# Kernel optimization log

Measured on AMD Instinct MI355X. Metric: run time of the kernel, lower is better.

Reference implementation:

```python
import jax, jax.numpy as jnp
import numpy as np

EPS = 1e-3  # kernel epsilon used in Performer generalized kernel
B, H, N, D, M = 1, 8, 1024, 64, 128  # batch, heads, seq, dim_heads, nb_features


def _gaussian_orthogonal_matrix(m, d, seed=0):
    # GaussianOrthogonalRandomMatrix with scaling=0: stacked QR blocks, rows
    # rescaled by chi-distributed norms of gaussian d-vectors.
    rng = np.random.default_rng(seed)
    blocks = []
    for _ in range(m // d):
        g = rng.standard_normal((d, d))
        qmat, _ = np.linalg.qr(g)
        blocks.append(qmat.T)
    proj = np.concatenate(blocks, axis=0)  # [m, d], orthonormal rows per block
    mult = np.linalg.norm(rng.standard_normal((m, d)), axis=1)  # chi norms
    return (mult[:, None] * proj).astype(np.float32)


def setup_inputs() -> dict:
    key = jax.random.key(0)
    kq, kk, kv = jax.random.split(key, 3)
    q = jax.random.normal(kq, (B, H, N, D), dtype=jnp.float32)
    k = jax.random.normal(kk, (B, H, N, D), dtype=jnp.float32)
    v = jax.random.normal(kv, (B, H, N, D), dtype=jnp.float32)
    proj = jnp.asarray(_gaussian_orthogonal_matrix(M, D))
    return {"q": q, "k": k, "v": v, "proj": proj}


def _generalized_kernel(x, proj):
    # kernel_fn(relu)( (x / d**0.25) @ proj^T ) + eps
    normalizer = 1.0 / (x.shape[-1] ** 0.25)
    xp = jnp.einsum('bhnd,md->bhnm', x * normalizer, proj)
    return jax.nn.relu(xp) + EPS


def reference(q, k, v, proj):
    qp = _generalized_kernel(q, proj)  # [B,H,N,M]
    kp = _generalized_kernel(k, proj)  # [B,H,N,M]
    # causal linear attention
    k_cumsum = jnp.cumsum(kp, axis=-2)                              # [B,H,N,M]
    context = jnp.einsum('bhnm,bhne->bhnme', kp, v)                 # [B,H,N,M,D]
    context = jnp.cumsum(context, axis=-3)                          # prefix sums over n
    context = context / k_cumsum[..., None]                         # normalize
    out = jnp.einsum('bhnme,bhnm->bhne', context, qp)               # [B,H,N,D]
    return out
```

## Files before the change

kernel.cpp:

```cpp
#include <hip/hip_runtime.h>

static constexpr int H = 8, N = 1024, D = 64, M = 128, CHUNK = 128, NC = 8;
static constexpr float EPS = 1e-3f;
static constexpr float NORM = 0.35355339059327373f;

typedef __attribute__((ext_vector_type(8))) short short8;
typedef __attribute__((ext_vector_type(4))) float f32x4;

__device__ inline unsigned short f2bf(float x) {
    unsigned u = __float_as_uint(x);
    return (unsigned short)((u + 0x7fffu + ((u >> 16) & 1u)) >> 16);
}
__device__ inline float bf2f(unsigned short u) {
    return __uint_as_float(((unsigned)u) << 16);
}
__device__ inline ushort4 pack4(float4 g) {
    return (ushort4){f2bf(g.x), f2bf(g.y), f2bf(g.z), f2bf(g.w)};
}

__global__ __launch_bounds__(512) void k_projg(const float* __restrict__ q,
                                               const float* __restrict__ k,
                                               const float* __restrict__ proj,
                                               const float* __restrict__ v,
                                               unsigned short* __restrict__ qpb,
                                               unsigned short* __restrict__ kpb,
                                               unsigned short* __restrict__ Gpb,
                                               float* __restrict__ kpart) {
    __shared__ __align__(16) short smem[30208];
    short* projb = smem;
    short* xb = smem + 9216;
    short* obuf = smem + 13824;
    short* kpT = smem + 22528;
    short* vT = smem + 27648;
    const int tid = threadIdx.x;
    const int rblk = blockIdx.x;
    const int h = blockIdx.y;
    const int rowbase = h * N + rblk * 32;
    const int lane = tid & 63, wv = tid >> 6;
    const int rt = wv & 3, mh = wv >> 2;
    const int fr = lane & 15, fq = lane >> 4;

    for (int i4 = tid; i4 < 2048; i4 += 512) {
        int m = i4 >> 4, dq = i4 & 15;
        *(ushort4*)&projb[m * 72 + dq * 4] = pack4(*(const float4*)&proj[i4 * 4]);
    }
    {
        int r = tid >> 4, dq = tid & 15;
        float4 g = *(const float4*)&q[(rowbase + r) * D + dq * 4];
        g.x *= NORM; g.y *= NORM; g.z *= NORM; g.w *= NORM;
        *(ushort4*)&xb[r * 72 + dq * 4] = pack4(g);
        float4 gk = *(const float4*)&k[(rowbase + r) * D + dq * 4];
        gk.x *= NORM; gk.y *= NORM; gk.z *= NORM; gk.w *= NORM;
        *(ushort4*)&xb[(32 + r) * 72 + dq * 4] = pack4(gk);
        int rv = tid & 31, e4 = (tid >> 5) * 4;
        float4 gv = *(const float4*)&v[(rowbase + rv) * D + e4];
        vT[(e4 + 0) * 40 + rv] = (short)f2bf(gv.x);
        vT[(e4 + 1) * 40 + rv] = (short)f2bf(gv.y);
        vT[(e4 + 2) * 40 + rv] = (short)f2bf(gv.z);
        vT[(e4 + 3) * 40 + rv] = (short)f2bf(gv.w);
    }
    __syncthreads();

    f32x4 accp[4];
#pragma unroll
    for (int i = 0; i < 4; i++) accp[i] = (f32x4){0.f, 0.f, 0.f, 0.f};
#pragma unroll
    for (int kt = 0; kt < 2; kt++) {
        short8 a = *(const short8*)&xb[(16 * rt + fr) * 72 + kt * 32 + fq * 8];
#pragma unroll
        for (int i = 0; i < 4; i++) {
            const int mt = mh * 4 + i;
            short8 bb = *(const short8*)&projb[(16 * mt + fr) * 72 + kt * 32 + fq * 8];
            accp[i] = __builtin_amdgcn_mfma_f32_16x16x32_bf16(a, bb, accp[i], 0, 0, 0);
        }
    }
#pragma unroll
    for (int i = 0; i < 4; i++) {
        const int mt = mh * 4 + i;
#pragma unroll
        for (int reg = 0; reg < 4; reg++) {
            const int r = 16 * rt + fq * 4 + reg;
            const int m = 16 * mt + fr;
            unsigned short bv = f2bf(fmaxf(accp[i][reg], 0.f) + EPS);
            obuf[r * 136 + m] = (short)bv;
            if (rt >= 2) kpT[m * 40 + (r - 32)] = (short)bv;
        }
    }
    __syncthreads();

    for (int i = tid; i < 2048; i += 512) {
        int r = i >> 5, cu = i & 31;
        ushort4 val = *(const ushort4*)&obuf[r * 136 + cu * 4];
        unsigned short* g = (r < 32) ? &qpb[(rowbase + r) * M + cu * 4]
                                     : &kpb[(rowbase + r - 32) * M + cu * 4];
        *(ushort4*)g = val;
    }
    const int gb = h * 32 + rblk;
    if (tid < 128) {
        float ks = 0.f;
#pragma unroll 8
        for (int r = 0; r < 32; r++) ks += bf2f((unsigned short)kpT[tid * 40 + r]);
        kpart[gb * M + tid] = ks;
    }
    __syncthreads();

    f32x4 gacc[4];
#pragma unroll
    for (int et = 0; et < 4; et++) gacc[et] = (f32x4){0.f, 0.f, 0.f, 0.f};
    {
        short8 a = *(const short8*)&kpT[(16 * wv + fr) * 40 + fq * 8];
#pragma unroll
        for (int et = 0; et < 4; et++) {
            short8 bb = *(const short8*)&vT[(16 * et + fr) * 40 + fq * 8];
            gacc[et] = __builtin_amdgcn_mfma_f32_16x16x32_bf16(a, bb, gacc[et], 0, 0, 0);
        }
    }
#pragma unroll
    for (int et = 0; et < 4; et++)
#pragma unroll
        for (int reg = 0; reg < 4; reg++) {
            const int m = 16 * wv + fq * 4 + reg;
            obuf[m * 68 + 16 * et + fr] = (short)f2bf(gacc[et][reg]);
        }
    __syncthreads();
    for (int i = tid; i < 2048; i += 512) {
        int m = i >> 4, e4 = (i & 15) * 4;
        *(ushort4*)&Gpb[(gb * M + m) * D + e4] = *(const ushort4*)&obuf[m * 68 + e4];
    }
}

__global__ __launch_bounds__(256) void k_prefix(const float* __restrict__ kpart,
                                                const unsigned short* __restrict__ Gpb,
                                                float* __restrict__ zpre,
                                                unsigned short* __restrict__ S0pre) {
    const int h = blockIdx.x >> 3, oct = blockIdx.x & 7;
    const int tid = threadIdx.x;
    const int eb = oct * 1024 + tid * 4;
    float a0 = 0.f, a1 = 0.f, a2 = 0.f, a3 = 0.f;
#pragma unroll
    for (int c = 0; c < 8; c++) {
        ushort4 w = {f2bf(a0), f2bf(a1), f2bf(a2), f2bf(a3)};
        *(ushort4*)&S0pre[(h * 8 + c) * (M * D) + eb] = w;
#pragma unroll
        for (int p = 0; p < 4; p++) {
            ushort4 g = *(const ushort4*)&Gpb[(h * 32 + c * 4 + p) * (M * D) + eb];
            a0 += bf2f(g.x);
            a1 += bf2f(g.y);
            a2 += bf2f(g.z);
            a3 += bf2f(g.w);
        }
    }
    if (oct == 0 && tid < 128) {
        float vals[32];
#pragma unroll
        for (int s = 0; s < 32; s++) vals[s] = kpart[(h * 32 + s) * M + tid];
        float z = 0.f;
#pragma unroll
        for (int s = 0; s < 32; s++) {
            zpre[(h * 32 + s) * M + tid] = z;
            z += vals[s];
        }
    }
}

__global__ __launch_bounds__(512) void k_attn(const unsigned short* __restrict__ qpb,
                                              const unsigned short* __restrict__ kpb,
                                              const float* __restrict__ zpre,
                                              const unsigned short* __restrict__ S0pre,
                                              const float* __restrict__ v,
                                              float* __restrict__ out) {
    __shared__ __align__(16) short smem[26112];
    short* bufA = smem;
    short* bufB = smem + 4352;
    short* bufC = smem + 21760;
    short* s0t = bufB;
    short* vT = bufB + 8704;
    const int tid = threadIdx.x;
    const int b = blockIdx.x;
    const int sub = blockIdx.y;
    const int h = b >> 3, c = 7 - (b & 7);
    const int chunkbase = h * N + c * CHUNK;
    const int rowstart = chunkbase + sub * 32;
    const int jrows = (sub + 1) * 32;
    const int lane = tid & 63, wv = tid >> 6;
    const int rt = wv & 1, js = wv >> 1;
    const int fr = lane & 15, fq = lane >> 4;

    float4 vpre[4];
#pragma unroll
    for (int t = 0; t < 4; t++) {
        const int i = tid + t * 512;
        const int j = i >> 4, e4 = (i & 15) * 4;
        vpre[t] = *(const float4*)&v[(chunkbase + j) * D + e4];
    }
    const int pm = tid >> 2, peb = (tid & 3) * 16;
    short8 s0a = *(const short8*)&S0pre[(h * 8 + c) * (M * D) + pm * D + peb];
    short8 s0b = *(const short8*)&S0pre[(h * 8 + c) * (M * D) + pm * D + peb + 8];
    float zinit = 0.f;
    if (tid < 128) zinit = zpre[(h * 32 + c * 4 + sub) * M + tid];

    {
        const unsigned int* src = (const unsigned int*)kpb;
        for (int i = tid; i < jrows * 64; i += 512) {
            int j = i >> 6, mu = i & 63;
            ((unsigned int*)&bufB[j * 136])[mu] = src[(chunkbase + j) * 64 + mu];
        }
        const unsigned int* srcq = (const unsigned int*)qpb;
        for (int i = tid; i < 2048; i += 512) {
            int r = i >> 6, mu = i & 63;
            ((unsigned int*)&bufC[r * 136])[mu] = srcq[(rowstart + r) * 64 + mu];
        }
    }
    __syncthreads();

    if (tid < 128) {
        const int m = tid;
        float z = zinit;
#pragma unroll 8
        for (int r = 0; r < 32; r++) {
            z += bf2f((unsigned short)bufB[(sub * 32 + r) * 136 + m]);
            bufA[r * 136 + m] = (short)f2bf(
                bf2f((unsigned short)bufC[r * 136 + m]) * __builtin_amdgcn_rcpf(z));
        }
    }
    __syncthreads();

    const int jtmax = 2 * sub + 2;
    f32x4 acc1[2];
    acc1[0] = (f32x4){0.f, 0.f, 0.f, 0.f};
    acc1[1] = (f32x4){0.f, 0.f, 0.f, 0.f};
#pragma unroll
    for (int kt = 0; kt < 4; kt++) {
        short8 a = *(const short8*)&bufA[(16 * rt + fr) * 136 + kt * 32 + fq * 8];
#pragma unroll
        for (int jl = 0; jl < 2; jl++) {
            const int jt = 2 * js + jl;
            if (jt < jtmax) {
                short8 bb =
                    *(const short8*)&bufB[(16 * jt + fr) * 136 + kt * 32 + fq * 8];
                acc1[jl] =
                    __builtin_amdgcn_mfma_f32_16x16x32_bf16(a, bb, acc1[jl], 0, 0, 0);
            }
        }
    }
    __syncthreads();

#pragma unroll
    for (int jl = 0; jl < 2; jl++) {
        const int jt = 2 * js + jl;
        if (jt < jtmax) {
            const int j = 16 * jt + fr;
#pragma unroll
            for (int reg = 0; reg < 4; reg++) {
                const int nloc = 16 * rt + fq * 4 + reg;
                float val = (j <= sub * 32 + nloc) ? acc1[jl][reg] : 0.f;
                bufC[nloc * 136 + j] = (short)f2bf(val);
            }
        }
    }
    {
#pragma unroll
        for (int j = 0; j < 8; j++) {
            s0t[(peb + j) * 136 + pm] = s0a[j];
            s0t[(peb + 8 + j) * 136 + pm] = s0b[j];
        }
    }
#pragma unroll
    for (int t = 0; t < 4; t++) {
        const int i = tid + t * 512;
        const int j = i >> 4, e4 = (i & 15) * 4;
        vT[(e4 + 0) * 136 + j] = (short)f2bf(vpre[t].x);
        vT[(e4 + 1) * 136 + j] = (short)f2bf(vpre[t].y);
        vT[(e4 + 2) * 136 + j] = (short)f2bf(vpre[t].z);
        vT[(e4 + 3) * 136 + j] = (short)f2bf(vpre[t].w);
    }
    __syncthreads();

    f32x4 acc2 = (f32x4){0.f, 0.f, 0.f, 0.f};
#pragma unroll
    for (int kt = 0; kt < 4; kt++) {
        short8 a = *(const short8*)&bufA[(16 * rt + fr) * 136 + kt * 32 + fq * 8];
        short8 bb = *(const short8*)&s0t[(16 * js + fr) * 136 + kt * 32 + fq * 8];
        acc2 = __builtin_amdgcn_mfma_f32_16x16x32_bf16(a, bb, acc2, 0, 0, 0);
    }
    const int ktmax = sub + 1;
    for (int kt = 0; kt < ktmax; kt++) {
        short8 a = *(const short8*)&bufC[(16 * rt + fr) * 136 + kt * 32 + fq * 8];
        short8 bb = *(const short8*)&vT[(16 * js + fr) * 136 + kt * 32 + fq * 8];
        acc2 = __builtin_amdgcn_mfma_f32_16x16x32_bf16(a, bb, acc2, 0, 0, 0);
    }

#pragma unroll
    for (int reg = 0; reg < 4; reg++) {
        out[(rowstart + 16 * rt + fq * 4 + reg) * D + 16 * js + fr] = acc2[reg];
    }
}

extern "C" void kernel_launch(void* const* d_in, const int* in_sizes, int n_in,
                              void* d_out, int out_size, void* d_ws, size_t ws_size,
                              hipStream_t stream) {
    const float* q = (const float*)d_in[0];
    const float* k = (const float*)d_in[1];
    const float* v = (const float*)d_in[2];
    const float* proj = (const float*)d_in[3];
    float* out = (float*)d_out;

    float* ws = (float*)d_ws;
    float* kpart = ws;
    unsigned short* qpb = (unsigned short*)(kpart + H * 32 * M);
    unsigned short* kpb = qpb + H * N * M;
    unsigned short* Gpb = kpb + H * N * M;
    float* zpre = (float*)(Gpb + H * 32 * M * D);
    unsigned short* S0pre = (unsigned short*)(zpre + H * 32 * M);

    k_projg<<<dim3(32, H), 512, 0, stream>>>(q, k, proj, v, qpb, kpb, Gpb,
                                             kpart);
    k_prefix<<<dim3(64), 256, 0, stream>>>(kpart, Gpb, zpre, S0pre);
    k_attn<<<dim3(H * NC, 4), 512, 0, stream>>>(qpb, kpb, zpre, S0pre, v, out);
}
```

Before: 81.16 us.

## Switch causal attention to 32-row chunks with per-subchunk state prefixes

The prefix kernel now emits a state prefix for every 32-row subchunk instead of every 128-row chunk. Each attention block then handles only its own 32 rows: a 32x32 intra-chunk causal product plus a state product, with no redundant loading of earlier rows within the chunk. This removes the uneven per-block work and the large key loads, at the cost of four times more S0pre prefix data written and read from global memory. The launch grid changes from 64x4 to 256 one-dimensional blocks.

```diff
diff --git a/kernel.cpp b/kernel.cpp
--- a/kernel.cpp
+++ b/kernel.cpp
@@ -1,6 +1,6 @@
 #include <hip/hip_runtime.h>
 
-static constexpr int H = 8, N = 1024, D = 64, M = 128, CHUNK = 128, NC = 8;
+static constexpr int H = 8, N = 1024, D = 64, M = 128;
 static constexpr float EPS = 1e-3f;
 static constexpr float NORM = 0.35355339059327373f;
 
@@ -137,18 +137,15 @@
     const int tid = threadIdx.x;
     const int eb = oct * 1024 + tid * 4;
     float a0 = 0.f, a1 = 0.f, a2 = 0.f, a3 = 0.f;
-#pragma unroll
-    for (int c = 0; c < 8; c++) {
+#pragma unroll 4
+    for (int s = 0; s < 32; s++) {
         ushort4 w = {f2bf(a0), f2bf(a1), f2bf(a2), f2bf(a3)};
-        *(ushort4*)&S0pre[(h * 8 + c) * (M * D) + eb] = w;
-#pragma unroll
-        for (int p = 0; p < 4; p++) {
-            ushort4 g = *(const ushort4*)&Gpb[(h * 32 + c * 4 + p) * (M * D) + eb];
-            a0 += bf2f(g.x);
-            a1 += bf2f(g.y);
-            a2 += bf2f(g.z);
-            a3 += bf2f(g.w);
-        }
+        *(ushort4*)&S0pre[(h * 32 + s) * (M * D) + eb] = w;
+        ushort4 g = *(const ushort4*)&Gpb[(h * 32 + s) * (M * D) + eb];
+        a0 += bf2f(g.x);
+        a1 += bf2f(g.y);
+        a2 += bf2f(g.z);
+        a3 += bf2f(g.w);
     }
     if (oct == 0 && tid < 128) {
         float vals[32];
@@ -169,48 +166,51 @@
                                               const unsigned short* __restrict__ S0pre,
                                               const float* __restrict__ v,
                                               float* __restrict__ out) {
-    __shared__ __align__(16) short smem[26112];
-    short* bufA = smem;
-    short* bufB = smem + 4352;
-    short* bufC = smem + 21760;
-    short* s0t = bufB;
-    short* vT = bufB + 8704;
+    __shared__ __align__(16) short smem[25600];
+    short* bufW = smem;
+    short* bufK = smem + 4352;
+    short* bufQ = smem + 8704;
+    short* s0t  = smem + 13056;
+    short* vT   = smem + 21760;
+    short* bufP = smem + 24320;
     const int tid = threadIdx.x;
     const int b = blockIdx.x;
-    const int sub = blockIdx.y;
-    const int h = b >> 3, c = 7 - (b & 7);
-    const int chunkbase = h * N + c * CHUNK;
-    const int rowstart = chunkbase + sub * 32;
-    const int jrows = (sub + 1) * 32;
+    const int h = b >> 5, s = b & 31;
+    const int rowstart = h * N + s * 32;
     const int lane = tid & 63, wv = tid >> 6;
     const int rt = wv & 1, js = wv >> 1;
     const int fr = lane & 15, fq = lane >> 4;
 
-    float4 vpre[4];
-#pragma unroll
-    for (int t = 0; t < 4; t++) {
-        const int i = tid + t * 512;
-        const int j = i >> 4, e4 = (i & 15) * 4;
-        vpre[t] = *(const float4*)&v[(chunkbase + j) * D + e4];
-    }
-    const int pm = tid >> 2, peb = (tid & 3) * 16;
-    short8 s0a = *(const short8*)&S0pre[(h * 8 + c) * (M * D) + pm * D + peb];
-    short8 s0b = *(const short8*)&S0pre[(h * 8 + c) * (M * D) + pm * D + peb + 8];
-    float zinit = 0.f;
-    if (tid < 128) zinit = zpre[(h * 32 + c * 4 + sub) * M + tid];
-
-    {
-        const unsigned int* src = (const unsigned int*)kpb;
-        for (int i = tid; i < jrows * 64; i += 512) {
-            int j = i >> 6, mu = i & 63;
-            ((unsigned int*)&bufB[j * 136])[mu] = src[(chunkbase + j) * 64 + mu];
-        }
+    {
+        const unsigned int* srck = (const unsigned int*)kpb;
         const unsigned int* srcq = (const unsigned int*)qpb;
         for (int i = tid; i < 2048; i += 512) {
-            int r = i >> 6, mu = i & 63;
-            ((unsigned int*)&bufC[r * 136])[mu] = srcq[(rowstart + r) * 64 + mu];
-        }
-    }
+            int j = i >> 6, mu = i & 63;
+            ((unsigned int*)&bufK[j * 136])[mu] = srck[(rowstart + j) * 64 + mu];
+            ((unsigned int*)&bufQ[j * 136])[mu] = srcq[(rowstart + j) * 64 + mu];
+        }
+    }
+    {
+        const int pm = tid >> 2, peb = (tid & 3) * 16;
+        const unsigned short* src = &S0pre[(h * 32 + s) * (M * D) + pm * D + peb];
+        short8 s0a = *(const short8*)&src[0];
+        short8 s0b = *(const short8*)&src[8];
+#pragma unroll
+        for (int j = 0; j < 8; j++) {
+            s0t[(peb + j) * 136 + pm] = s0a[j];
+            s0t[(peb + 8 + j) * 136 + pm] = s0b[j];
+        }
+    }
+    {
+        const int j = tid >> 4, e4 = (tid & 15) * 4;
+        float4 gv = *(const float4*)&v[(rowstart + j) * D + e4];
+        vT[(e4 + 0) * 40 + j] = (short)f2bf(gv.x);
+        vT[(e4 + 1) * 40 + j] = (short)f2bf(gv.y);
+        vT[(e4 + 2) * 40 + j] = (short)f2bf(gv.z);
+        vT[(e4 + 3) * 40 + j] = (short)f2bf(gv.w);
+    }
+    float zinit = 0.f;
+    if (tid < 128) zinit = zpre[(h * 32 + s) * M + tid];
     __syncthreads();
 
     if (tid < 128) {
@@ -218,75 +218,42 @@
         float z = zinit;
 #pragma unroll 8
         for (int r = 0; r < 32; r++) {
-            z += bf2f((unsigned short)bufB[(sub * 32 + r) * 136 + m]);
-            bufA[r * 136 + m] = (short)f2bf(
-                bf2f((unsigned short)bufC[r * 136 + m]) * __builtin_amdgcn_rcpf(z));
-        }
-    }
-    __syncthreads();
-
-    const int jtmax = 2 * sub + 2;
-    f32x4 acc1[2];
-    acc1[0] = (f32x4){0.f, 0.f, 0.f, 0.f};
-    acc1[1] = (f32x4){0.f, 0.f, 0.f, 0.f};
+            z += bf2f((unsigned short)bufK[r * 136 + m]);
+            bufW[r * 136 + m] = (short)f2bf(
+                bf2f((unsigned short)bufQ[r * 136 + m]) * __builtin_amdgcn_rcpf(z));
+        }
+    }
+    __syncthreads();
+
+    f32x4 acc2 = (f32x4){0.f, 0.f, 0.f, 0.f};
 #pragma unroll
     for (int kt = 0; kt < 4; kt++) {
-        short8 a = *(const short8*)&bufA[(16 * rt + fr) * 136 + kt * 32 + fq * 8];
-#pragma unroll
-        for (int jl = 0; jl < 2; jl++) {
-            const int jt = 2 * js + jl;
-            if (jt < jtmax) {
-                short8 bb =
-                    *(const short8*)&bufB[(16 * jt + fr) * 136 + kt * 32 + fq * 8];
-                acc1[jl] =
-                    __builtin_amdgcn_mfma_f32_16x16x32_bf16(a, bb, acc1[jl], 0, 0, 0);
-            }
-        }
-    }
-    __syncthreads();
-
-#pragma unroll
-    for (int jl = 0; jl < 2; jl++) {
-        const int jt = 2 * js + jl;
-        if (jt < jtmax) {
-            const int j = 16 * jt + fr;
-#pragma unroll
-            for (int reg = 0; reg < 4; reg++) {
-                const int nloc = 16 * rt + fq * 4 + reg;
-                float val = (j <= sub * 32 + nloc) ? acc1[jl][reg] : 0.f;
-                bufC[nloc * 136 + j] = (short)f2bf(val);
-            }
-        }
-    }
-    {
-#pragma unroll
-        for (int j = 0; j < 8; j++) {
-            s0t[(peb + j) * 136 + pm] = s0a[j];
-            s0t[(peb + 8 + j) * 136 + pm] = s0b[j];
-        }
-    }
-#pragma unroll
-    for (int t = 0; t < 4; t++) {
-        const int i = tid + t * 512;
-        const int j = i >> 4, e4 = (i & 15) * 4;
-        vT[(e4 + 0) * 136 + j] = (short)f2bf(vpre[t].x);
-        vT[(e4 + 1) * 136 + j] = (short)f2bf(vpre[t].y);
-        vT[(e4 + 2) * 136 + j] = (short)f2bf(vpre[t].z);
-        vT[(e4 + 3) * 136 + j] = (short)f2bf(vpre[t].w);
-    }
-    __syncthreads();
-
-    f32x4 acc2 = (f32x4){0.f, 0.f, 0.f, 0.f};
-#pragma unroll
-    for (int kt = 0; kt < 4; kt++) {
-        short8 a = *(const short8*)&bufA[(16 * rt + fr) * 136 + kt * 32 + fq * 8];
+        short8 a = *(const short8*)&bufW[(16 * rt + fr) * 136 + kt * 32 + fq * 8];
         short8 bb = *(const short8*)&s0t[(16 * js + fr) * 136 + kt * 32 + fq * 8];
         acc2 = __builtin_amdgcn_mfma_f32_16x16x32_bf16(a, bb, acc2, 0, 0, 0);
     }
-    const int ktmax = sub + 1;
-    for (int kt = 0; kt < ktmax; kt++) {
-        short8 a = *(const short8*)&bufC[(16 * rt + fr) * 136 + kt * 32 + fq * 8];
-        short8 bb = *(const short8*)&vT[(16 * js + fr) * 136 + kt * 32 + fq * 8];
+    if (wv < 4) {
+        const int jt = wv >> 1;
+        f32x4 acc1 = (f32x4){0.f, 0.f, 0.f, 0.f};
+#pragma unroll
+        for (int kt = 0; kt < 4; kt++) {
+            short8 a = *(const short8*)&bufW[(16 * rt + fr) * 136 + kt * 32 + fq * 8];
+            short8 bb = *(const short8*)&bufK[(16 * jt + fr) * 136 + kt * 32 + fq * 8];
+            acc1 = __builtin_amdgcn_mfma_f32_16x16x32_bf16(a, bb, acc1, 0, 0, 0);
+        }
+        const int j = 16 * jt + fr;
+#pragma unroll
+        for (int reg = 0; reg < 4; reg++) {
+            const int nloc = 16 * rt + fq * 4 + reg;
+            float val = (j <= nloc) ? acc1[reg] : 0.f;
+            bufP[nloc * 40 + j] = (short)f2bf(val);
+        }
+    }
+    __syncthreads();
+
+    {
+        short8 a = *(const short8*)&bufP[(16 * rt + fr) * 40 + fq * 8];
+        short8 bb = *(const short8*)&vT[(16 * js + fr) * 40 + fq * 8];
         acc2 = __builtin_amdgcn_mfma_f32_16x16x32_bf16(a, bb, acc2, 0, 0, 0);
     }
 
@@ -316,5 +283,5 @@
     k_projg<<<dim3(32, H), 512, 0, stream>>>(q, k, proj, v, qpb, kpb, Gpb,
                                              kpart);
     k_prefix<<<dim3(64), 256, 0, stream>>>(kpart, Gpb, zpre, S0pre);
-    k_attn<<<dim3(H * NC, 4), 512, 0, stream>>>(qpb, kpb, zpre, S0pre, v, out);
-}
+    k_attn<<<dim3(H * 32), 512, 0, stream>>>(qpb, kpb, zpre, S0pre, v, out);
+}
```

Measured after the change: 80.30 us. Within noise of the previous version (-1.1%).
